# Kernel tuning notes

Hardware: AMD Instinct MI355X
Metric: run time of the kernel (lower is better)

## Reference

```python
import jax, jax.numpy as jnp
import numpy as np

N, D, E, K = 16384, 4096, 128, 2

def setup_inputs() -> dict:
    key = jax.random.key(0)
    k1, k2 = jax.random.split(key)
    x = jax.random.normal(k1, (N, D), dtype=jnp.float32)
    W = jax.random.normal(k2, (E, D), dtype=jnp.float32) * (1.0 / np.sqrt(D))
    b = jnp.zeros((E,), dtype=jnp.float32)
    return {"x": x, "W": W, "b": b}

def reference(x, W, b):
    # logits = x @ W.T + b  -> [N, E]
    logits = jnp.einsum('nd,ed->ne', x, W) + b
    confidence = jax.nn.sigmoid(logits)
    top_k_vals, top_k_indices = jax.lax.top_k(confidence, K)  # [N, K]
    return top_k_vals, top_k_indices
```

## Files before the change

kernel.cpp:

```cpp
#include <hip/hip_runtime.h>
#include <stdint.h>
#include <math.h>

#define N_ROWS 16384
#define D_DIM  4096
#define E_EXP  128
#define BM     32
#define BKR    128
#define KSPLIT 2
#define KCHUNK (D_DIM / KSPLIT)
#define NR     (KCHUNK / BKR)
#define TAU    2.5e-4f

typedef short  short8 __attribute__((ext_vector_type(8)));
typedef float  f32x4  __attribute__((ext_vector_type(4)));

__device__ __forceinline__ uint32_t bf16_rne(float f) {
  uint32_t u = __builtin_bit_cast(uint32_t, f);
  return (u + 0x7fffu + ((u >> 16) & 1u)) >> 16;
}

__global__ __launch_bounds__(256) void k0_split(const float* __restrict__ W,
                                                uint16_t* __restrict__ wt) {
  const int b  = blockIdx.x;
  const int t  = threadIdx.x;
  const int eg  = b >> 5;
  const int kcg = b & 31;
  const int kc  = kcg * 4 + (t >> 6);
  const int lane = t & 63;
  const int e  = eg * 16 + (lane & 15);
  const int k0 = kc * 32 + (lane >> 4) * 8;

  const float* src = W + (size_t)e * D_DIM + k0;
  f32x4 w0 = *(const f32x4*)src;
  f32x4 w1 = *(const f32x4*)(src + 4);
  float wf[8] = {w0[0], w0[1], w0[2], w0[3], w1[0], w1[1], w1[2], w1[3]};

  uint16_t h[8], l[8];
  #pragma unroll
  for (int j = 0; j < 8; ++j) {
    uint32_t hh = bf16_rne(wf[j]);
    float hf = __builtin_bit_cast(float, hh << 16);
    h[j] = (uint16_t)hh;
    l[j] = (uint16_t)bf16_rne(wf[j] - hf);
  }
  const size_t blkh = ((size_t)(eg * 128 + kc) * 2 + 0) * 512;
  const size_t blkl = ((size_t)(eg * 128 + kc) * 2 + 1) * 512;
  *(short8*)(wt + blkh + lane * 8) = *(const short8*)h;
  *(short8*)(wt + blkl + lane * 8) = *(const short8*)l;
}

__global__ __launch_bounds__(512, 8) void k1_main(
    const float* __restrict__ x, const uint16_t* __restrict__ wt,
    float* __restrict__ part)
{
  __shared__ __align__(16) uint8_t smem[32768];

  const int t    = threadIdx.x;
  const int lane = t & 63;
  const int wv   = __builtin_amdgcn_readfirstlane(t >> 6);
  const int bid  = blockIdx.x;
  const int rt   = bid >> 1;
  const int ks   = bid & 1;
  const int row0 = rt * BM;
  const int kb0  = ks * KCHUNK;

  const int srow = t >> 4;
  const int skg  = t & 15;
  const float* xp = x + (size_t)(row0 + srow) * D_DIM + kb0 + skg * 8;

  const int s_w = skg >> 2, gg_w = skg & 3, rr_w = srow & 15, rg_w = srow >> 4;
  const int p_w  = gg_w * 16 + (rr_w ^ (gg_w << 1) ^ s_w);
  const int wa_h = (s_w * 4 + rg_w * 2 + 0) * 1024 + p_w * 16;
  const int wa_l = wa_h + 1024;

  const int ggr = lane >> 4, rrr = lane & 15;
  const int p_r0 = ggr * 16 + (rrr ^ (ggr << 1));

  const short8* Wt8 = (const short8*)wt;
  const int ccol = lane & 15;

  f32x4 acc[2] = {};

  f32x4 xa0, xa1, xb0, xb1;
  xa0 = *((const f32x4*)xp + 0); xa1 = *((const f32x4*)xp + 1);
  xb0 = *((const f32x4*)(xp + BKR) + 0); xb1 = *((const f32x4*)(xp + BKR) + 1);

  #pragma unroll 2
  for (int r = 0; r < NR; ++r) {
    float xf[8] = {xa0[0], xa0[1], xa0[2], xa0[3], xa1[0], xa1[1], xa1[2], xa1[3]};
    uint32_t hpk[4], lpk[4];
    #pragma unroll
    for (int j = 0; j < 4; ++j) {
      uint32_t h0 = bf16_rne(xf[2*j]), h1 = bf16_rne(xf[2*j+1]);
      float h0f = __builtin_bit_cast(float, h0 << 16);
      float h1f = __builtin_bit_cast(float, h1 << 16);
      uint32_t l0 = bf16_rne(xf[2*j] - h0f), l1 = bf16_rne(xf[2*j+1] - h1f);
      hpk[j] = h0 | (h1 << 16);
      lpk[j] = l0 | (l1 << 16);
    }
    uint8_t* buf = smem + (r & 1) * 16384;
    *(uint4*)(buf + wa_h) = make_uint4(hpk[0], hpk[1], hpk[2], hpk[3]);
    *(uint4*)(buf + wa_l) = make_uint4(lpk[0], lpk[1], lpk[2], lpk[3]);

    xa0 = xb0; xa1 = xb1;
    if (r + 2 < NR) {
      const f32x4* np = (const f32x4*)(xp + (size_t)(r + 2) * BKR);
      xb0 = np[0]; xb1 = np[1];
    }

    asm volatile("s_waitcnt lgkmcnt(0)" ::: "memory");
    __builtin_amdgcn_s_barrier();

    #pragma unroll
    for (int s = 0; s < 4; ++s) {
      const int pr = p_r0 ^ s;
      const int kcc = ks * (KCHUNK / 32) + r * 4 + s;
      const size_t bb = ((size_t)(wv * 128 + kcc) * 2) * 64 + lane;
      const short8 bh = Wt8[bb];
      const short8 bl = Wt8[bb + 64];
      #pragma unroll
      for (int rg = 0; rg < 2; ++rg) {
        const uint8_t* fb = buf + (s * 4 + rg * 2) * 1024 + pr * 16;
        short8 ah = *(const short8*)fb;
        short8 al = *(const short8*)(fb + 1024);
        acc[rg] = __builtin_amdgcn_mfma_f32_16x16x32_bf16(ah, bh, acc[rg], 0, 0, 0);
        acc[rg] = __builtin_amdgcn_mfma_f32_16x16x32_bf16(al, bh, acc[rg], 0, 0, 0);
        acc[rg] = __builtin_amdgcn_mfma_f32_16x16x32_bf16(ah, bl, acc[rg], 0, 0, 0);
      }
    }
  }

  float* dst = part + ((size_t)ks * N_ROWS + row0) * E_EXP;
  #pragma unroll
  for (int rg = 0; rg < 2; ++rg)
    #pragma unroll
    for (int i = 0; i < 4; ++i) {
      int row = rg * 16 + ggr * 4 + i;
      int e = wv * 16 + ccol;
      dst[(size_t)row * E_EXP + e] = acc[rg][i];
    }
}

__global__ __launch_bounds__(512) void k3_reduce(
    const float* __restrict__ part, const float* __restrict__ bias,
    float* __restrict__ out, int* __restrict__ flags)
{
  const int t = threadIdx.x;
  const int row = t >> 4, prt = t & 15;
  const int grow = blockIdx.x * 32 + row;
  const float* pp = part + (size_t)grow * E_EXP + prt * 8;

  f32x4 s0 = {}, s1 = {};
  #pragma unroll
  for (int ks = 0; ks < KSPLIT; ++ks) {
    const float* q = pp + (size_t)ks * N_ROWS * E_EXP;
    f32x4 a = *(const f32x4*)q;
    f32x4 b = *(const f32x4*)(q + 4);
    s0 += a; s1 += b;
  }
  float lv[8] = {s0[0], s0[1], s0[2], s0[3], s1[0], s1[1], s1[2], s1[3]};

  float l1 = -3e38f, l2 = -3e38f, l3 = -3e38f;
  int   i1 = -1, i2 = -1, i3 = -1;
  auto ins = [&](float v, int e) {
    if (v > l1 || (v == l1 && e < i1)) { l3=l2; i3=i2; l2=l1; i2=i1; l1=v; i1=e; }
    else if (v > l2 || (v == l2 && e < i2)) { l3=l2; i3=i2; l2=v; i2=e; }
    else if (v > l3 || (v == l3 && e < i3)) { l3=v; i3=e; }
  };
  #pragma unroll
  for (int j = 0; j < 8; ++j) {
    int e = prt * 8 + j;
    ins(lv[j] + bias[e], e);
  }
  #pragma unroll
  for (int m = 1; m <= 8; m <<= 1) {
    float a1 = __shfl_xor(l1, m), a2 = __shfl_xor(l2, m), a3 = __shfl_xor(l3, m);
    int   b1i = __shfl_xor(i1, m), b2i = __shfl_xor(i2, m), b3i = __shfl_xor(i3, m);
    ins(a1, b1i); ins(a2, b2i); ins(a3, b3i);
  }
  if (prt == 0) {
    int fl = ((l1 - l2) < TAU) || ((l2 - l3) < TAU);
    flags[grow] = fl;
    out[(size_t)grow * 2 + 0] = 1.f / (1.f + __expf(-l1));
    out[(size_t)grow * 2 + 1] = 1.f / (1.f + __expf(-l2));
    out[(size_t)N_ROWS * 2 + (size_t)grow * 2 + 0] = (float)i1;
    out[(size_t)N_ROWS * 2 + (size_t)grow * 2 + 1] = (float)i2;
  }
}

__global__ __launch_bounds__(1024) void k2_fix(
    const float* __restrict__ x, const float* __restrict__ W,
    const float* __restrict__ bias, const int* __restrict__ flags,
    float* __restrict__ out)
{
  __shared__ double lgs[E_EXP];
  const int t    = threadIdx.x;
  const int wvi  = t >> 6, lane = t & 63;
  const int e    = wvi * 8 + (lane >> 3);
  const int sub  = lane & 7;
  const int rbase = blockIdx.x * 8;

  for (int rr = 0; rr < 8; ++rr) {
    const int row = rbase + rr;
    if (!flags[row]) continue;
    const float* xr = x + (size_t)row * D_DIM;
    const float* wr = W + (size_t)e * D_DIM;
    double a0 = 0.0, a1 = 0.0, a2 = 0.0, a3 = 0.0;
    for (int j = 0; j < 128; ++j) {
      const int c4 = (j * 8 + sub) * 4;
      f32x4 xv = *(const f32x4*)(xr + c4);
      f32x4 wvv = *(const f32x4*)(wr + c4);
      a0 += (double)xv[0] * wvv[0];
      a1 += (double)xv[1] * wvv[1];
      a2 += (double)xv[2] * wvv[2];
      a3 += (double)xv[3] * wvv[3];
    }
    double acc = (a0 + a1) + (a2 + a3);
    #pragma unroll
    for (int m = 1; m <= 4; m <<= 1) acc += __shfl_xor(acc, m);
    if (sub == 0) lgs[e] = acc + (double)bias[e];
    __syncthreads();
    if (t == 0) {
      double l1 = -1e300, l2 = -1e300; int i1 = -1, i2 = -1;
      for (int ee = 0; ee < E_EXP; ++ee) {
        double v = lgs[ee];
        if (v > l1) { l2 = l1; i2 = i1; l1 = v; i1 = ee; }
        else if (v > l2) { l2 = v; i2 = ee; }
      }
      out[(size_t)row * 2 + 0] = (float)(1.0 / (1.0 + exp(-l1)));
      out[(size_t)row * 2 + 1] = (float)(1.0 / (1.0 + exp(-l2)));
      out[(size_t)N_ROWS * 2 + (size_t)row * 2 + 0] = (float)i1;
      out[(size_t)N_ROWS * 2 + (size_t)row * 2 + 1] = (float)i2;
    }
    __syncthreads();
  }
}

extern "C" void kernel_launch(void* const* d_in, const int* in_sizes, int n_in,
                              void* d_out, int out_size, void* d_ws, size_t ws_size,
                              hipStream_t stream) {
  const float* x  = (const float*)d_in[0];
  const float* Wm = (const float*)d_in[1];
  const float* b  = (const float*)d_in[2];
  float* out = (float*)d_out;

  uint16_t* wt   = (uint16_t*)d_ws;
  int*      flags = (int*)((uint8_t*)d_ws + 2u * 1024 * 1024);
  float*    part = (float*)((uint8_t*)d_ws + 4u * 1024 * 1024);

  k0_split<<<dim3(256), dim3(256), 0, stream>>>(Wm, wt);
  k1_main<<<dim3((N_ROWS / BM) * KSPLIT), dim3(512), 0, stream>>>(x, wt, part);
  k3_reduce<<<dim3(N_ROWS / 32), dim3(512), 0, stream>>>(part, b, out, flags);
  k2_fix<<<dim3(N_ROWS / 8), dim3(1024), 0, stream>>>(x, Wm, b, flags, out);
}
```

Baseline: 190.2 us.

## Pre-tile x to bf16-high only, drop K-split, widen fp64 fix-up tolerance

Adds a pre-pass that converts x into MFMA-fragment-ordered bf16, keeping only the high part, and staging it through LDS with global_load_lds. The main GEMM then streams fragments straight from global memory without LDS or barriers. It computes 32x32 output tiles per wave with 2 MFMAs per pair (x_hi*W_hi, x_hi*W_lo) instead of 3, and drops the K-split and partial-sum reduction. Because dropping x_lo costs precision, the near-tie tolerance TAU rises from 2.5e-4 to 2e-2, so many more rows go to the fp64 fix-up kernel. That adds extra traffic for the bf16 copy of x and more fix-up work in return.

Result: slower. 674.4 us (+254.7%).

```diff
diff --git a/kernel.cpp b/kernel.cpp
--- a/kernel.cpp
+++ b/kernel.cpp
@@ -5,15 +5,17 @@
 #define N_ROWS 16384
 #define D_DIM  4096
 #define E_EXP  128
-#define BM     32
-#define BKR    128
-#define KSPLIT 2
-#define KCHUNK (D_DIM / KSPLIT)
-#define NR     (KCHUNK / BKR)
-#define TAU    2.5e-4f
+#define TAU    2.0e-2f
 
 typedef short  short8 __attribute__((ext_vector_type(8)));
 typedef float  f32x4  __attribute__((ext_vector_type(4)));
+
+#define GAS __attribute__((address_space(1)))
+#define LAS __attribute__((address_space(3)))
+
+__device__ __forceinline__ void g2lds16(const float* g, uint8_t* l) {
+  __builtin_amdgcn_global_load_lds((const GAS uint32_t*)g, (LAS uint32_t*)l, 16, 0, 0);
+}
 
 __device__ __forceinline__ uint32_t bf16_rne(float f) {
   uint32_t u = __builtin_bit_cast(uint32_t, f);
@@ -50,116 +52,106 @@
   *(short8*)(wt + blkl + lane * 8) = *(const short8*)l;
 }
 
-__global__ __launch_bounds__(512, 8) void k1_main(
-    const float* __restrict__ x, const uint16_t* __restrict__ wt,
-    float* __restrict__ part)
+__global__ __launch_bounds__(512) void k0x_tile(const float* __restrict__ x,
+                                                uint16_t* __restrict__ tx) {
+  __shared__ __align__(16) uint8_t smem[65536];
+  float* Lx = (float*)smem;
+
+  const int bid  = blockIdx.x;
+  const int rt16 = bid >> 2;
+  const int kh   = bid & 3;
+  const int t    = threadIdx.x;
+
+  const int prow = t >> 8, pk = (t & 255) * 4;
+  #pragma unroll
+  for (int i = 0; i < 8; ++i) {
+    const float* src = x + (size_t)(rt16 * 16 + i * 2 + prow) * D_DIM + kh * 1024 + pk;
+    g2lds16(src, smem + i * 8192 + t * 16);
+  }
+  asm volatile("s_waitcnt vmcnt(0)" ::: "memory");
+  __syncthreads();
+
+  const int fi = t >> 4, sub = t & 15;
+  const size_t fragbase = ((size_t)rt16 * 128 + kh * 32 + fi) * 512;
+  #pragma unroll
+  for (int i = 0; i < 4; ++i) {
+    const int li  = sub * 4 + i;
+    const int row = li & 15, kg = li >> 4;
+    const float* rp = Lx + row * 1024 + fi * 32 + kg * 8;
+    f32x4 a = *(const f32x4*)rp;
+    f32x4 b = *(const f32x4*)(rp + 4);
+    uint16_t h[8];
+    h[0] = (uint16_t)bf16_rne(a[0]); h[1] = (uint16_t)bf16_rne(a[1]);
+    h[2] = (uint16_t)bf16_rne(a[2]); h[3] = (uint16_t)bf16_rne(a[3]);
+    h[4] = (uint16_t)bf16_rne(b[0]); h[5] = (uint16_t)bf16_rne(b[1]);
+    h[6] = (uint16_t)bf16_rne(b[2]); h[7] = (uint16_t)bf16_rne(b[3]);
+    *(short8*)(tx + fragbase + li * 8) = *(const short8*)h;
+  }
+}
+
+__global__ __launch_bounds__(512) void k1_main(
+    const uint16_t* __restrict__ tx, const uint16_t* __restrict__ wt,
+    float* __restrict__ lg)
 {
-  __shared__ __align__(16) uint8_t smem[32768];
-
   const int t    = threadIdx.x;
   const int lane = t & 63;
   const int wv   = __builtin_amdgcn_readfirstlane(t >> 6);
-  const int bid  = blockIdx.x;
-  const int rt   = bid >> 1;
-  const int ks   = bid & 1;
-  const int row0 = rt * BM;
-  const int kb0  = ks * KCHUNK;
-
-  const int srow = t >> 4;
-  const int skg  = t & 15;
-  const float* xp = x + (size_t)(row0 + srow) * D_DIM + kb0 + skg * 8;
-
-  const int s_w = skg >> 2, gg_w = skg & 3, rr_w = srow & 15, rg_w = srow >> 4;
-  const int p_w  = gg_w * 16 + (rr_w ^ (gg_w << 1) ^ s_w);
-  const int wa_h = (s_w * 4 + rg_w * 2 + 0) * 1024 + p_w * 16;
-  const int wa_l = wa_h + 1024;
-
-  const int ggr = lane >> 4, rrr = lane & 15;
-  const int p_r0 = ggr * 16 + (rrr ^ (ggr << 1));
-
-  const short8* Wt8 = (const short8*)wt;
-  const int ccol = lane & 15;
-
-  f32x4 acc[2] = {};
-
-  f32x4 xa0, xa1, xb0, xb1;
-  xa0 = *((const f32x4*)xp + 0); xa1 = *((const f32x4*)xp + 1);
-  xb0 = *((const f32x4*)(xp + BKR) + 0); xb1 = *((const f32x4*)(xp + BKR) + 1);
-
-  #pragma unroll 2
-  for (int r = 0; r < NR; ++r) {
-    float xf[8] = {xa0[0], xa0[1], xa0[2], xa0[3], xa1[0], xa1[1], xa1[2], xa1[3]};
-    uint32_t hpk[4], lpk[4];
-    #pragma unroll
-    for (int j = 0; j < 4; ++j) {
-      uint32_t h0 = bf16_rne(xf[2*j]), h1 = bf16_rne(xf[2*j+1]);
-      float h0f = __builtin_bit_cast(float, h0 << 16);
-      float h1f = __builtin_bit_cast(float, h1 << 16);
-      uint32_t l0 = bf16_rne(xf[2*j] - h0f), l1 = bf16_rne(xf[2*j+1] - h1f);
-      hpk[j] = h0 | (h1 << 16);
-      lpk[j] = l0 | (l1 << 16);
-    }
-    uint8_t* buf = smem + (r & 1) * 16384;
-    *(uint4*)(buf + wa_h) = make_uint4(hpk[0], hpk[1], hpk[2], hpk[3]);
-    *(uint4*)(buf + wa_l) = make_uint4(lpk[0], lpk[1], lpk[2], lpk[3]);
-
-    xa0 = xb0; xa1 = xb1;
-    if (r + 2 < NR) {
-      const f32x4* np = (const f32x4*)(xp + (size_t)(r + 2) * BKR);
-      xb0 = np[0]; xb1 = np[1];
-    }
-
-    asm volatile("s_waitcnt lgkmcnt(0)" ::: "memory");
-    __builtin_amdgcn_s_barrier();
-
-    #pragma unroll
-    for (int s = 0; s < 4; ++s) {
-      const int pr = p_r0 ^ s;
-      const int kcc = ks * (KCHUNK / 32) + r * 4 + s;
-      const size_t bb = ((size_t)(wv * 128 + kcc) * 2) * 64 + lane;
-      const short8 bh = Wt8[bb];
-      const short8 bl = Wt8[bb + 64];
-      #pragma unroll
-      for (int rg = 0; rg < 2; ++rg) {
-        const uint8_t* fb = buf + (s * 4 + rg * 2) * 1024 + pr * 16;
-        short8 ah = *(const short8*)fb;
-        short8 al = *(const short8*)(fb + 1024);
-        acc[rg] = __builtin_amdgcn_mfma_f32_16x16x32_bf16(ah, bh, acc[rg], 0, 0, 0);
-        acc[rg] = __builtin_amdgcn_mfma_f32_16x16x32_bf16(al, bh, acc[rg], 0, 0, 0);
-        acc[rg] = __builtin_amdgcn_mfma_f32_16x16x32_bf16(ah, bl, acc[rg], 0, 0, 0);
-      }
-    }
-  }
-
-  float* dst = part + ((size_t)ks * N_ROWS + row0) * E_EXP;
+  const int wj   = blockIdx.x * 8 + wv;
+  const int rt   = wj >> 2;
+  const int eq   = wj & 3;
+
+  const short8* X8 = (const short8*)tx;
+  const short8* W8 = (const short8*)wt;
+  const size_t xb0 = ((size_t)(rt * 2 + 0) * 128) * 64 + lane;
+  const size_t xb1 = ((size_t)(rt * 2 + 1) * 128) * 64 + lane;
+  const size_t wb0 = ((size_t)((eq * 2 + 0) * 128) * 2) * 64 + lane;
+  const size_t wb1 = ((size_t)((eq * 2 + 1) * 128) * 2) * 64 + lane;
+
+  f32x4 acc[2][2] = {};
+
+  #pragma unroll 4
+  for (int kc = 0; kc < 128; ++kc) {
+    short8 a0  = X8[xb0 + (size_t)kc * 64];
+    short8 a1  = X8[xb1 + (size_t)kc * 64];
+    short8 bh0 = W8[wb0 + (size_t)(kc * 2 + 0) * 64];
+    short8 bl0 = W8[wb0 + (size_t)(kc * 2 + 1) * 64];
+    short8 bh1 = W8[wb1 + (size_t)(kc * 2 + 0) * 64];
+    short8 bl1 = W8[wb1 + (size_t)(kc * 2 + 1) * 64];
+    acc[0][0] = __builtin_amdgcn_mfma_f32_16x16x32_bf16(a0, bh0, acc[0][0], 0, 0, 0);
+    acc[0][0] = __builtin_amdgcn_mfma_f32_16x16x32_bf16(a0, bl0, acc[0][0], 0, 0, 0);
+    acc[0][1] = __builtin_amdgcn_mfma_f32_16x16x32_bf16(a0, bh1, acc[0][1], 0, 0, 0);
+    acc[0][1] = __builtin_amdgcn_mfma_f32_16x16x32_bf16(a0, bl1, acc[0][1], 0, 0, 0);
+    acc[1][0] = __builtin_amdgcn_mfma_f32_16x16x32_bf16(a1, bh0, acc[1][0], 0, 0, 0);
+    acc[1][0] = __builtin_amdgcn_mfma_f32_16x16x32_bf16(a1, bl0, acc[1][0], 0, 0, 0);
+    acc[1][1] = __builtin_amdgcn_mfma_f32_16x16x32_bf16(a1, bh1, acc[1][1], 0, 0, 0);
+    acc[1][1] = __builtin_amdgcn_mfma_f32_16x16x32_bf16(a1, bl1, acc[1][1], 0, 0, 0);
+  }
+
+  const int ggr = lane >> 4, ccol = lane & 15;
   #pragma unroll
   for (int rg = 0; rg < 2; ++rg)
     #pragma unroll
-    for (int i = 0; i < 4; ++i) {
-      int row = rg * 16 + ggr * 4 + i;
-      int e = wv * 16 + ccol;
-      dst[(size_t)row * E_EXP + e] = acc[rg][i];
-    }
+    for (int egi = 0; egi < 2; ++egi)
+      #pragma unroll
+      for (int i = 0; i < 4; ++i) {
+        int row = rt * 32 + rg * 16 + ggr * 4 + i;
+        int e   = eq * 32 + egi * 16 + ccol;
+        lg[(size_t)row * E_EXP + e] = acc[rg][egi][i];
+      }
 }
 
 __global__ __launch_bounds__(512) void k3_reduce(
-    const float* __restrict__ part, const float* __restrict__ bias,
+    const float* __restrict__ lg, const float* __restrict__ bias,
     float* __restrict__ out, int* __restrict__ flags)
 {
   const int t = threadIdx.x;
   const int row = t >> 4, prt = t & 15;
   const int grow = blockIdx.x * 32 + row;
-  const float* pp = part + (size_t)grow * E_EXP + prt * 8;
-
-  f32x4 s0 = {}, s1 = {};
-  #pragma unroll
-  for (int ks = 0; ks < KSPLIT; ++ks) {
-    const float* q = pp + (size_t)ks * N_ROWS * E_EXP;
-    f32x4 a = *(const f32x4*)q;
-    f32x4 b = *(const f32x4*)(q + 4);
-    s0 += a; s1 += b;
-  }
-  float lv[8] = {s0[0], s0[1], s0[2], s0[3], s1[0], s1[1], s1[2], s1[3]};
+  const float* pp = lg + (size_t)grow * E_EXP + prt * 8;
+
+  f32x4 a = *(const f32x4*)pp;
+  f32x4 b = *(const f32x4*)(pp + 4);
+  float lv[8] = {a[0], a[1], a[2], a[3], b[0], b[1], b[2], b[3]};
 
   float l1 = -3e38f, l2 = -3e38f, l3 = -3e38f;
   int   i1 = -1, i2 = -1, i3 = -1;
@@ -199,9 +191,9 @@
   const int wvi  = t >> 6, lane = t & 63;
   const int e    = wvi * 8 + (lane >> 3);
   const int sub  = lane & 7;
-  const int rbase = blockIdx.x * 8;
-
-  for (int rr = 0; rr < 8; ++rr) {
+  const int rbase = blockIdx.x * 4;
+
+  for (int rr = 0; rr < 4; ++rr) {
     const int row = rbase + rr;
     if (!flags[row]) continue;
     const float* xr = x + (size_t)row * D_DIM;
@@ -245,12 +237,15 @@
   const float* b  = (const float*)d_in[2];
   float* out = (float*)d_out;
 
-  uint16_t* wt   = (uint16_t*)d_ws;
-  int*      flags = (int*)((uint8_t*)d_ws + 2u * 1024 * 1024);
-  float*    part = (float*)((uint8_t*)d_ws + 4u * 1024 * 1024);
+  uint8_t* ws = (uint8_t*)d_ws;
+  uint16_t* wt    = (uint16_t*)ws;
+  int*      flags = (int*)(ws + 2u * 1024 * 1024);
+  uint16_t* tx    = (uint16_t*)(ws + 4u * 1024 * 1024);
+  float*    lgts  = (float*)(ws + 4u * 1024 * 1024 + 134217728u);
 
   k0_split<<<dim3(256), dim3(256), 0, stream>>>(Wm, wt);
-  k1_main<<<dim3((N_ROWS / BM) * KSPLIT), dim3(512), 0, stream>>>(x, wt, part);
-  k3_reduce<<<dim3(N_ROWS / 32), dim3(512), 0, stream>>>(part, b, out, flags);
-  k2_fix<<<dim3(N_ROWS / 8), dim3(1024), 0, stream>>>(x, Wm, b, flags, out);
-}
+  k0x_tile<<<dim3(4096), dim3(512), 0, stream>>>(x, tx);
+  k1_main<<<dim3(256), dim3(512), 0, stream>>>(tx, wt, lgts);
+  k3_reduce<<<dim3(N_ROWS / 32), dim3(512), 0, stream>>>(lgts, b, out, flags);
+  k2_fix<<<dim3(N_ROWS / 4), dim3(1024), 0, stream>>>(x, Wm, b, flags, out);
+}
```

## Drop LDS staging in GEMM kernel; each wave owns 16 rows across all experts

Applied to the files above, without the earlier changes.

The main logits kernel no longer stages split bf16 x tiles in shared memory behind barriers. Each wave now loads and splits its own 16 rows of x straight into MFMA operand registers and loops over all 8 expert groups, keeping 8 accumulators. The K split rises from 2 to 4 and the grid becomes 128 row groups by 4 K chunks. This removes LDS writes, reads and block barriers, but every wave now reads the full W slice for its K chunk, which raises W traffic through L2. It also doubles the partial-sum buffer that the reduce kernel has to read.

Result: slower. 315.3 us (+65.8%).

```diff
diff --git a/kernel.cpp b/kernel.cpp
--- a/kernel.cpp
+++ b/kernel.cpp
@@ -5,11 +5,9 @@
 #define N_ROWS 16384
 #define D_DIM  4096
 #define E_EXP  128
-#define BM     32
-#define BKR    128
-#define KSPLIT 2
+#define KSPLIT 4
 #define KCHUNK (D_DIM / KSPLIT)
-#define NR     (KCHUNK / BKR)
+#define NKC    (KCHUNK / 32)
 #define TAU    2.5e-4f
 
 typedef short  short8 __attribute__((ext_vector_type(8)));
@@ -50,45 +48,29 @@
   *(short8*)(wt + blkl + lane * 8) = *(const short8*)l;
 }
 
-__global__ __launch_bounds__(512, 8) void k1_main(
+__global__ __launch_bounds__(512, 4) void k1_main(
     const float* __restrict__ x, const uint16_t* __restrict__ wt,
     float* __restrict__ part)
 {
-  __shared__ __align__(16) uint8_t smem[32768];
-
   const int t    = threadIdx.x;
   const int lane = t & 63;
   const int wv   = __builtin_amdgcn_readfirstlane(t >> 6);
-  const int bid  = blockIdx.x;
-  const int rt   = bid >> 1;
-  const int ks   = bid & 1;
-  const int row0 = rt * BM;
-  const int kb0  = ks * KCHUNK;
-
-  const int srow = t >> 4;
-  const int skg  = t & 15;
-  const float* xp = x + (size_t)(row0 + srow) * D_DIM + kb0 + skg * 8;
-
-  const int s_w = skg >> 2, gg_w = skg & 3, rr_w = srow & 15, rg_w = srow >> 4;
-  const int p_w  = gg_w * 16 + (rr_w ^ (gg_w << 1) ^ s_w);
-  const int wa_h = (s_w * 4 + rg_w * 2 + 0) * 1024 + p_w * 16;
-  const int wa_l = wa_h + 1024;
-
-  const int ggr = lane >> 4, rrr = lane & 15;
-  const int p_r0 = ggr * 16 + (rrr ^ (ggr << 1));
-
-  const short8* Wt8 = (const short8*)wt;
-  const int ccol = lane & 15;
-
-  f32x4 acc[2] = {};
-
-  f32x4 xa0, xa1, xb0, xb1;
-  xa0 = *((const f32x4*)xp + 0); xa1 = *((const f32x4*)xp + 1);
-  xb0 = *((const f32x4*)(xp + BKR) + 0); xb1 = *((const f32x4*)(xp + BKR) + 1);
+  const int rg   = blockIdx.x >> 2;
+  const int kh   = blockIdx.x & 3;
+  const int row0 = rg * 128 + wv * 16;
+  const int r15  = lane & 15, kg = lane >> 4;
+
+  const float* xp = x + (size_t)(row0 + r15) * D_DIM + kh * KCHUNK + kg * 8;
+  const short8* W8 = (const short8*)wt;
+
+  f32x4 acc[8] = {};
 
   #pragma unroll 2
-  for (int r = 0; r < NR; ++r) {
-    float xf[8] = {xa0[0], xa0[1], xa0[2], xa0[3], xa1[0], xa1[1], xa1[2], xa1[3]};
+  for (int kc = 0; kc < NKC; ++kc) {
+    f32x4 a = *(const f32x4*)(xp + kc * 32);
+    f32x4 b = *(const f32x4*)(xp + kc * 32 + 4);
+    float xf[8] = {a[0], a[1], a[2], a[3], b[0], b[1], b[2], b[3]};
+
     uint32_t hpk[4], lpk[4];
     #pragma unroll
     for (int j = 0; j < 4; ++j) {
@@ -99,46 +81,28 @@
       hpk[j] = h0 | (h1 << 16);
       lpk[j] = l0 | (l1 << 16);
     }
-    uint8_t* buf = smem + (r & 1) * 16384;
-    *(uint4*)(buf + wa_h) = make_uint4(hpk[0], hpk[1], hpk[2], hpk[3]);
-    *(uint4*)(buf + wa_l) = make_uint4(lpk[0], lpk[1], lpk[2], lpk[3]);
-
-    xa0 = xb0; xa1 = xb1;
-    if (r + 2 < NR) {
-      const f32x4* np = (const f32x4*)(xp + (size_t)(r + 2) * BKR);
-      xb0 = np[0]; xb1 = np[1];
-    }
-
-    asm volatile("s_waitcnt lgkmcnt(0)" ::: "memory");
-    __builtin_amdgcn_s_barrier();
-
-    #pragma unroll
-    for (int s = 0; s < 4; ++s) {
-      const int pr = p_r0 ^ s;
-      const int kcc = ks * (KCHUNK / 32) + r * 4 + s;
-      const size_t bb = ((size_t)(wv * 128 + kcc) * 2) * 64 + lane;
-      const short8 bh = Wt8[bb];
-      const short8 bl = Wt8[bb + 64];
-      #pragma unroll
-      for (int rg = 0; rg < 2; ++rg) {
-        const uint8_t* fb = buf + (s * 4 + rg * 2) * 1024 + pr * 16;
-        short8 ah = *(const short8*)fb;
-        short8 al = *(const short8*)(fb + 1024);
-        acc[rg] = __builtin_amdgcn_mfma_f32_16x16x32_bf16(ah, bh, acc[rg], 0, 0, 0);
-        acc[rg] = __builtin_amdgcn_mfma_f32_16x16x32_bf16(al, bh, acc[rg], 0, 0, 0);
-        acc[rg] = __builtin_amdgcn_mfma_f32_16x16x32_bf16(ah, bl, acc[rg], 0, 0, 0);
-      }
-    }
-  }
-
-  float* dst = part + ((size_t)ks * N_ROWS + row0) * E_EXP;
-  #pragma unroll
-  for (int rg = 0; rg < 2; ++rg)
+    short8 ah = __builtin_bit_cast(short8, *(uint4*)hpk);
+    short8 al = __builtin_bit_cast(short8, *(uint4*)lpk);
+
+    const int kcg = kh * NKC + kc;
+    #pragma unroll
+    for (int eg = 0; eg < 8; ++eg) {
+      const size_t bb = ((size_t)(eg * 128 + kcg) * 2) * 64 + lane;
+      short8 bh = W8[bb];
+      short8 bl = W8[bb + 64];
+      acc[eg] = __builtin_amdgcn_mfma_f32_16x16x32_bf16(ah, bh, acc[eg], 0, 0, 0);
+      acc[eg] = __builtin_amdgcn_mfma_f32_16x16x32_bf16(al, bh, acc[eg], 0, 0, 0);
+      acc[eg] = __builtin_amdgcn_mfma_f32_16x16x32_bf16(ah, bl, acc[eg], 0, 0, 0);
+    }
+  }
+
+  float* dst = part + ((size_t)kh * N_ROWS + row0) * E_EXP;
+  #pragma unroll
+  for (int eg = 0; eg < 8; ++eg)
     #pragma unroll
     for (int i = 0; i < 4; ++i) {
-      int row = rg * 16 + ggr * 4 + i;
-      int e = wv * 16 + ccol;
-      dst[(size_t)row * E_EXP + e] = acc[rg][i];
+      int rl = kg * 4 + i;
+      dst[(size_t)rl * E_EXP + eg * 16 + r15] = acc[eg][i];
     }
 }
 
@@ -245,12 +209,13 @@
   const float* b  = (const float*)d_in[2];
   float* out = (float*)d_out;
 
-  uint16_t* wt   = (uint16_t*)d_ws;
-  int*      flags = (int*)((uint8_t*)d_ws + 2u * 1024 * 1024);
-  float*    part = (float*)((uint8_t*)d_ws + 4u * 1024 * 1024);
+  uint8_t* ws = (uint8_t*)d_ws;
+  uint16_t* wt    = (uint16_t*)ws;
+  int*      flags = (int*)(ws + 2u * 1024 * 1024);
+  float*    part  = (float*)(ws + 4u * 1024 * 1024);
 
   k0_split<<<dim3(256), dim3(256), 0, stream>>>(Wm, wt);
-  k1_main<<<dim3((N_ROWS / BM) * KSPLIT), dim3(512), 0, stream>>>(x, wt, part);
+  k1_main<<<dim3(128 * KSPLIT), dim3(512), 0, stream>>>(x, wt, part);
   k3_reduce<<<dim3(N_ROWS / 32), dim3(512), 0, stream>>>(part, b, out, flags);
   k2_fix<<<dim3(N_ROWS / 8), dim3(1024), 0, stream>>>(x, Wm, b, flags, out);
 }
```

## Double row tile to 64 and split waves across row halves and expert pairs

Applied to the files above, without the earlier changes.

The main GEMM block now covers 64 rows instead of 32. Its 8 waves are arranged as 2 row-halves by 4 expert-quarters, and each wave computes 2x2 MFMA tiles. Each W fragment loaded from global memory is therefore reused across twice as many rows, which halves W traffic per row and halves the number of blocks. In exchange, LDS per block doubles to 64 KB, launch bounds drop occupancy to 4, register pressure rises, and the grid has fewer blocks to spread over the CUs.

Result: no change. 192.2 us (+1.1%).

```diff
diff --git a/kernel.cpp b/kernel.cpp
--- a/kernel.cpp
+++ b/kernel.cpp
@@ -5,11 +5,11 @@
 #define N_ROWS 16384
 #define D_DIM  4096
 #define E_EXP  128
-#define BM     32
+#define BM     64
 #define BKR    128
 #define KSPLIT 2
 #define KCHUNK (D_DIM / KSPLIT)
-#define NR     (KCHUNK / BKR)
+#define NRND   (KCHUNK / BKR)
 #define TAU    2.5e-4f
 
 typedef short  short8 __attribute__((ext_vector_type(8)));
@@ -50,29 +50,30 @@
   *(short8*)(wt + blkl + lane * 8) = *(const short8*)l;
 }
 
-__global__ __launch_bounds__(512, 8) void k1_main(
+__global__ __launch_bounds__(512, 4) void k1_main(
     const float* __restrict__ x, const uint16_t* __restrict__ wt,
     float* __restrict__ part)
 {
-  __shared__ __align__(16) uint8_t smem[32768];
+  __shared__ __align__(16) uint8_t smem[65536];
 
   const int t    = threadIdx.x;
   const int lane = t & 63;
   const int wv   = __builtin_amdgcn_readfirstlane(t >> 6);
-  const int bid  = blockIdx.x;
-  const int rt   = bid >> 1;
-  const int ks   = bid & 1;
+  const int rh   = wv >> 2;
+  const int eq   = wv & 3;
+  const int rt   = blockIdx.x >> 1;
+  const int kh   = blockIdx.x & 1;
   const int row0 = rt * BM;
-  const int kb0  = ks * KCHUNK;
-
-  const int srow = t >> 4;
-  const int skg  = t & 15;
-  const float* xp = x + (size_t)(row0 + srow) * D_DIM + kb0 + skg * 8;
-
-  const int s_w = skg >> 2, gg_w = skg & 3, rr_w = srow & 15, rg_w = srow >> 4;
+  const int kb0  = kh * KCHUNK;
+
+  const int lr0 = t >> 4;
+  const int kg  = t & 15;
+  const float* xp0 = x + (size_t)(row0 + lr0) * D_DIM + kb0 + kg * 8;
+  const float* xp1 = xp0 + (size_t)32 * D_DIM;
+
+  const int s_w = kg >> 2, gg_w = kg & 3, rr_w = lr0 & 15, rg0 = lr0 >> 4;
   const int p_w  = gg_w * 16 + (rr_w ^ (gg_w << 1) ^ s_w);
-  const int wa_h = (s_w * 4 + rg_w * 2 + 0) * 1024 + p_w * 16;
-  const int wa_l = wa_h + 1024;
+  const int wa0h = (s_w * 8 + rg0 * 2 + 0) * 1024 + p_w * 16;
 
   const int ggr = lane >> 4, rrr = lane & 15;
   const int p_r0 = ggr * 16 + (rrr ^ (ggr << 1));
@@ -80,33 +81,42 @@
   const short8* Wt8 = (const short8*)wt;
   const int ccol = lane & 15;
 
-  f32x4 acc[2] = {};
-
-  f32x4 xa0, xa1, xb0, xb1;
-  xa0 = *((const f32x4*)xp + 0); xa1 = *((const f32x4*)xp + 1);
-  xb0 = *((const f32x4*)(xp + BKR) + 0); xb1 = *((const f32x4*)(xp + BKR) + 1);
+  f32x4 acc[2][2] = {};
+
+  f32x4 xa[4], xb[4];
+  xa[0] = *((const f32x4*)xp0 + 0); xa[1] = *((const f32x4*)xp0 + 1);
+  xa[2] = *((const f32x4*)xp1 + 0); xa[3] = *((const f32x4*)xp1 + 1);
+  xb[0] = *((const f32x4*)(xp0 + BKR) + 0); xb[1] = *((const f32x4*)(xp0 + BKR) + 1);
+  xb[2] = *((const f32x4*)(xp1 + BKR) + 0); xb[3] = *((const f32x4*)(xp1 + BKR) + 1);
 
   #pragma unroll 2
-  for (int r = 0; r < NR; ++r) {
-    float xf[8] = {xa0[0], xa0[1], xa0[2], xa0[3], xa1[0], xa1[1], xa1[2], xa1[3]};
-    uint32_t hpk[4], lpk[4];
-    #pragma unroll
-    for (int j = 0; j < 4; ++j) {
-      uint32_t h0 = bf16_rne(xf[2*j]), h1 = bf16_rne(xf[2*j+1]);
-      float h0f = __builtin_bit_cast(float, h0 << 16);
-      float h1f = __builtin_bit_cast(float, h1 << 16);
-      uint32_t l0 = bf16_rne(xf[2*j] - h0f), l1 = bf16_rne(xf[2*j+1] - h1f);
-      hpk[j] = h0 | (h1 << 16);
-      lpk[j] = l0 | (l1 << 16);
-    }
-    uint8_t* buf = smem + (r & 1) * 16384;
-    *(uint4*)(buf + wa_h) = make_uint4(hpk[0], hpk[1], hpk[2], hpk[3]);
-    *(uint4*)(buf + wa_l) = make_uint4(lpk[0], lpk[1], lpk[2], lpk[3]);
-
-    xa0 = xb0; xa1 = xb1;
-    if (r + 2 < NR) {
-      const f32x4* np = (const f32x4*)(xp + (size_t)(r + 2) * BKR);
-      xb0 = np[0]; xb1 = np[1];
+  for (int r = 0; r < NRND; ++r) {
+    uint8_t* buf = smem + (r & 1) * 32768;
+    #pragma unroll
+    for (int c = 0; c < 2; ++c) {
+      float xf[8] = {xa[c*2][0], xa[c*2][1], xa[c*2][2], xa[c*2][3],
+                     xa[c*2+1][0], xa[c*2+1][1], xa[c*2+1][2], xa[c*2+1][3]};
+      uint32_t hpk[4], lpk[4];
+      #pragma unroll
+      for (int j = 0; j < 4; ++j) {
+        uint32_t h0 = bf16_rne(xf[2*j]), h1 = bf16_rne(xf[2*j+1]);
+        float h0f = __builtin_bit_cast(float, h0 << 16);
+        float h1f = __builtin_bit_cast(float, h1 << 16);
+        uint32_t l0 = bf16_rne(xf[2*j] - h0f), l1 = bf16_rne(xf[2*j+1] - h1f);
+        hpk[j] = h0 | (h1 << 16);
+        lpk[j] = l0 | (l1 << 16);
+      }
+      *(uint4*)(buf + wa0h + c * 4096)        = make_uint4(hpk[0], hpk[1], hpk[2], hpk[3]);
+      *(uint4*)(buf + wa0h + c * 4096 + 1024) = make_uint4(lpk[0], lpk[1], lpk[2], lpk[3]);
+    }
+
+    #pragma unroll
+    for (int q = 0; q < 4; ++q) xa[q] = xb[q];
+    if (r + 2 < NRND) {
+      const float* n0 = xp0 + (size_t)(r + 2) * BKR;
+      const float* n1 = xp1 + (size_t)(r + 2) * BKR;
+      xb[0] = *((const f32x4*)n0 + 0); xb[1] = *((const f32x4*)n0 + 1);
+      xb[2] = *((const f32x4*)n1 + 0); xb[3] = *((const f32x4*)n1 + 1);
     }
 
     asm volatile("s_waitcnt lgkmcnt(0)" ::: "memory");
@@ -115,31 +125,38 @@
     #pragma unroll
     for (int s = 0; s < 4; ++s) {
       const int pr = p_r0 ^ s;
-      const int kcc = ks * (KCHUNK / 32) + r * 4 + s;
-      const size_t bb = ((size_t)(wv * 128 + kcc) * 2) * 64 + lane;
-      const short8 bh = Wt8[bb];
-      const short8 bl = Wt8[bb + 64];
+      const int kcg = kh * 64 + r * 4 + s;
       #pragma unroll
-      for (int rg = 0; rg < 2; ++rg) {
-        const uint8_t* fb = buf + (s * 4 + rg * 2) * 1024 + pr * 16;
-        short8 ah = *(const short8*)fb;
-        short8 al = *(const short8*)(fb + 1024);
-        acc[rg] = __builtin_amdgcn_mfma_f32_16x16x32_bf16(ah, bh, acc[rg], 0, 0, 0);
-        acc[rg] = __builtin_amdgcn_mfma_f32_16x16x32_bf16(al, bh, acc[rg], 0, 0, 0);
-        acc[rg] = __builtin_amdgcn_mfma_f32_16x16x32_bf16(ah, bl, acc[rg], 0, 0, 0);
-      }
-    }
-  }
-
-  float* dst = part + ((size_t)ks * N_ROWS + row0) * E_EXP;
+      for (int egi = 0; egi < 2; ++egi) {
+        const int eg8 = eq * 2 + egi;
+        const size_t bb = ((size_t)(eg8 * 128 + kcg) * 2) * 64 + lane;
+        const short8 bh = Wt8[bb];
+        const short8 bl = Wt8[bb + 64];
+        #pragma unroll
+        for (int rg = 0; rg < 2; ++rg) {
+          const int rgg = rh * 2 + rg;
+          const uint8_t* fb = buf + (s * 8 + rgg * 2) * 1024 + pr * 16;
+          short8 ah = *(const short8*)fb;
+          short8 al = *(const short8*)(fb + 1024);
+          acc[rg][egi] = __builtin_amdgcn_mfma_f32_16x16x32_bf16(ah, bh, acc[rg][egi], 0, 0, 0);
+          acc[rg][egi] = __builtin_amdgcn_mfma_f32_16x16x32_bf16(al, bh, acc[rg][egi], 0, 0, 0);
+          acc[rg][egi] = __builtin_amdgcn_mfma_f32_16x16x32_bf16(ah, bl, acc[rg][egi], 0, 0, 0);
+        }
+      }
+    }
+  }
+
+  float* dst = part + ((size_t)kh * N_ROWS + row0) * E_EXP;
   #pragma unroll
   for (int rg = 0; rg < 2; ++rg)
     #pragma unroll
-    for (int i = 0; i < 4; ++i) {
-      int row = rg * 16 + ggr * 4 + i;
-      int e = wv * 16 + ccol;
-      dst[(size_t)row * E_EXP + e] = acc[rg][i];
-    }
+    for (int egi = 0; egi < 2; ++egi)
+      #pragma unroll
+      for (int i = 0; i < 4; ++i) {
+        int rl = (rh * 2 + rg) * 16 + ggr * 4 + i;
+        int e  = (eq * 2 + egi) * 16 + ccol;
+        dst[(size_t)rl * E_EXP + e] = acc[rg][egi][i];
+      }
 }
 
 __global__ __launch_bounds__(512) void k3_reduce(
@@ -245,9 +262,10 @@
   const float* b  = (const float*)d_in[2];
   float* out = (float*)d_out;
 
-  uint16_t* wt   = (uint16_t*)d_ws;
-  int*      flags = (int*)((uint8_t*)d_ws + 2u * 1024 * 1024);
-  float*    part = (float*)((uint8_t*)d_ws + 4u * 1024 * 1024);
+  uint8_t* ws = (uint8_t*)d_ws;
+  uint16_t* wt    = (uint16_t*)ws;
+  int*      flags = (int*)(ws + 2u * 1024 * 1024);
+  float*    part  = (float*)(ws + 4u * 1024 * 1024);
 
   k0_split<<<dim3(256), dim3(256), 0, stream>>>(Wm, wt);
   k1_main<<<dim3((N_ROWS / BM) * KSPLIT), dim3(512), 0, stream>>>(x, wt, part);
```
